# Performance work log

Hardware: AMD Instinct MI355X
Metric: run time of the kernel (lower is better)

The kernel has to match this reference:

```python
import jax, jax.numpy as jnp
import numpy as np

N = 100000      # nodes
E = 1600000     # edges (before self-loops)
IN = 256        # in_channels
H = 4           # heads (layer 1)
C = 16          # hidden_channels
OUT = 40        # out_channels
NEG_SLOPE = 0.2  # PyG GATConv default


def setup_inputs() -> dict:
    key = jax.random.key(0)
    ks = jax.random.split(key, 10)
    x = jax.random.normal(ks[0], (N, IN), dtype=jnp.float32)
    edge_index = jax.random.randint(ks[1], (2, E), 0, N, dtype=jnp.int64)
    s = 0.1
    return {
        "x": x,
        "edge_index": edge_index,
        "W1": jax.random.normal(ks[2], (IN, H * C), dtype=jnp.float32) * s,
        "a_src1": jax.random.normal(ks[3], (H, C), dtype=jnp.float32) * s,
        "a_dst1": jax.random.normal(ks[4], (H, C), dtype=jnp.float32) * s,
        "b1": jnp.zeros((H * C,), dtype=jnp.float32),
        "W2": jax.random.normal(ks[5], (H * C, OUT), dtype=jnp.float32) * s,
        "a_src2": jax.random.normal(ks[6], (1, OUT), dtype=jnp.float32) * s,
        "a_dst2": jax.random.normal(ks[7], (1, OUT), dtype=jnp.float32) * s,
        "b2": jnp.zeros((OUT,), dtype=jnp.float32),
    }


def gat_conv(x, src, dst, W, a_s, a_d, b, heads, ch, n):
    # x: [n, d_in] -> projected [n, heads, ch]
    xp = (x @ W).reshape(n, heads, ch)
    # per-node attention contributions [n, heads]
    e_s = jnp.einsum('nhc,hc->nh', xp, a_s)
    e_d = jnp.einsum('nhc,hc->nh', xp, a_d)
    # per-edge logits (gather) [E, heads]
    e = jax.nn.leaky_relu(e_s[src] + e_d[dst], negative_slope=NEG_SLOPE)
    # segment softmax over edges sharing a destination node
    m = jax.ops.segment_max(e, dst, num_segments=n)
    m = jnp.where(jnp.isfinite(m), m, 0.0)
    ex = jnp.exp(e - m[dst])
    z = jax.ops.segment_sum(ex, dst, num_segments=n)
    alpha = ex / (z[dst] + 1e-16)               # [E, heads]
    # weighted scatter-add aggregation [n, heads, ch]
    out = jax.ops.segment_sum(xp[src] * alpha[:, :, None], dst, num_segments=n)
    return out.reshape(n, heads * ch) + b       # concat heads + bias


def reference(x, edge_index, W1, a_src1, a_dst1, b1, W2, a_src2, a_dst2, b2):
    n = x.shape[0]
    loop = jnp.arange(n, dtype=edge_index.dtype)
    src = jnp.concatenate([edge_index[0], loop])  # PyG add_self_loops=True
    dst = jnp.concatenate([edge_index[1], loop])
    h = gat_conv(x, src, dst, W1, a_src1, a_dst1, b1, H, C, n)
    h = jax.nn.relu(h)
    out = gat_conv(h, src, dst, W2, a_src2, a_dst2, b2, 1, OUT, n)
    return out
```

## Files before the change

kernel.cpp:

```cpp
#include <hip/hip_runtime.h>
#include <hip/hip_bf16.h>

#define IN_DIM 256
#define HC     64
#define OUT_DIM 40
#define NEG    0.2f

#define NB_SH   8
#define NB_MASK 255
#define SRC_BITS 17
#define SRC_MASK 0x1FFFF
#define CHUNK   8192
#define LEN_CAP 6144

typedef __bf16 bf16x8 __attribute__((ext_vector_type(8)));
typedef float  f32x4  __attribute__((ext_vector_type(4)));

__device__ inline float lrelu(float v) { return fmaxf(v, NEG * v); }

__global__ __launch_bounds__(256) void hist_kernel(
    const int* __restrict__ ei, int* __restrict__ blkhistT, int* __restrict__ btot,
    int E, int ET, int nbuck, int nblk) {
  __shared__ int hist[512];
  int tid = threadIdx.x;
  hist[tid] = 0; hist[tid + 256] = 0;
  __syncthreads();
  int base = blockIdx.x * CHUNK;
  #pragma unroll
  for (int it = 0; it < CHUNK / 1024; ++it) {
    int e = base + it * 1024 + tid * 4;
    if (e + 3 < E) {
      int4 d4 = *(const int4*)&ei[E + e];
      atomicAdd(&hist[d4.x >> NB_SH], 1);
      atomicAdd(&hist[d4.y >> NB_SH], 1);
      atomicAdd(&hist[d4.z >> NB_SH], 1);
      atomicAdd(&hist[d4.w >> NB_SH], 1);
    } else {
      #pragma unroll
      for (int k = 0; k < 4; ++k) {
        int ee = e + k;
        if (ee < ET) {
          int d = (ee < E) ? ei[E + ee] : (ee - E);
          atomicAdd(&hist[d >> NB_SH], 1);
        }
      }
    }
  }
  __syncthreads();
  for (int i = tid; i < nbuck; i += 256) {
    int c = hist[i];
    blkhistT[(size_t)i * nblk + blockIdx.x] = c;
    if (c) atomicAdd(&btot[i], c);
  }
}

__global__ __launch_bounds__(512) void bscan_kernel(
    const int* __restrict__ btot, int* __restrict__ bstart,
    int* __restrict__ offs, int nbuck, int ET, int n) {
  __shared__ int sm[512];
  int tid = threadIdx.x;
  int total = (tid < nbuck) ? btot[tid] : 0;
  sm[tid] = total; __syncthreads();
  for (int o = 1; o < 512; o <<= 1) {
    int v = (tid >= o) ? sm[tid - o] : 0;
    __syncthreads();
    sm[tid] += v;
    __syncthreads();
  }
  if (tid < nbuck) bstart[tid] = sm[tid] - total;
  if (tid == 0) { bstart[nbuck] = ET; offs[n] = ET; }
}

__global__ __launch_bounds__(256) void curs_kernel(
    const int* __restrict__ blkhistT, const int* __restrict__ bstart,
    int* __restrict__ cur, int nblk, int nbuck) {
  __shared__ int sm[256];
  int b = blockIdx.x, tid = threadIdx.x;
  int run = bstart[b];
  for (int c = 0; c < nblk; c += 256) {
    int idx = c + tid;
    int v = (idx < nblk) ? blkhistT[(size_t)b * nblk + idx] : 0;
    sm[tid] = v; __syncthreads();
    for (int o = 1; o < 256; o <<= 1) {
      int x = (tid >= o) ? sm[tid - o] : 0;
      __syncthreads();
      sm[tid] += x;
      __syncthreads();
    }
    if (idx < nblk) cur[(size_t)idx * nbuck + b] = run + sm[tid] - v;
    run += sm[255];
    __syncthreads();
  }
}

__global__ __launch_bounds__(512) void scatter1_kernel(
    const int* __restrict__ ei, const int* __restrict__ cur,
    unsigned int* __restrict__ pairs, int E, int ET, int nbuck) {
  __shared__ int hs[512];
  __shared__ int addb[512];
  __shared__ int lcnt[512];
  __shared__ unsigned int lout[CHUNK];
  __shared__ int ldst[CHUNK];
  int tid = threadIdx.x, blk = blockIdx.x, base = blk * CHUNK;
  hs[tid] = 0; lcnt[tid] = 0;
  __syncthreads();
  int se[16], de[16];
  #pragma unroll
  for (int it = 0; it < CHUNK / 2048; ++it) {
    int e = base + it * 2048 + tid * 4;
    if (e + 3 < E) {
      int4 s4 = *(const int4*)&ei[e];
      int4 d4 = *(const int4*)&ei[E + e];
      se[it * 4 + 0] = s4.x; de[it * 4 + 0] = d4.x; atomicAdd(&hs[d4.x >> NB_SH], 1);
      se[it * 4 + 1] = s4.y; de[it * 4 + 1] = d4.y; atomicAdd(&hs[d4.y >> NB_SH], 1);
      se[it * 4 + 2] = s4.z; de[it * 4 + 2] = d4.z; atomicAdd(&hs[d4.z >> NB_SH], 1);
      se[it * 4 + 3] = s4.w; de[it * 4 + 3] = d4.w; atomicAdd(&hs[d4.w >> NB_SH], 1);
    } else {
      #pragma unroll
      for (int k = 0; k < 4; ++k) {
        int ee = e + k;
        int s = 0, d = 0;
        if (ee < ET) {
          if (ee < E) { s = ei[ee]; d = ei[E + ee]; }
          else        { s = ee - E; d = s; }
          atomicAdd(&hs[d >> NB_SH], 1);
        }
        se[it * 4 + k] = s; de[it * 4 + k] = d;
      }
    }
  }
  __syncthreads();
  int t = hs[tid];
  for (int o = 1; o < 512; o <<= 1) {
    int v = (tid >= o) ? hs[tid - o] : 0;
    __syncthreads();
    hs[tid] += v;
    __syncthreads();
  }
  int lofs = hs[tid] - t;
  __syncthreads();
  hs[tid] = lofs;
  addb[tid] = ((tid < nbuck) ? cur[(size_t)blk * nbuck + tid] : 0) - lofs;
  __syncthreads();
  #pragma unroll
  for (int it = 0; it < CHUNK / 2048; ++it) {
    #pragma unroll
    for (int k = 0; k < 4; ++k) {
      int e = base + it * 2048 + tid * 4 + k;
      if (e < ET) {
        int b = de[it * 4 + k] >> NB_SH;
        int pos = hs[b] + atomicAdd(&lcnt[b], 1);
        lout[pos] = (unsigned)se[it * 4 + k] |
                    ((unsigned)(de[it * 4 + k] & NB_MASK) << SRC_BITS);
        ldst[pos] = addb[b] + pos;
      }
    }
  }
  __syncthreads();
  int len = min(CHUNK, ET - base);
  for (int i = tid; i < len; i += 512) pairs[ldst[i]] = lout[i];
}

__global__ __launch_bounds__(512) void place2_kernel(
    const unsigned int* __restrict__ pairs, const int* __restrict__ bstart,
    int* __restrict__ offs, int* __restrict__ srcs, int n, int nbuck) {
  __shared__ unsigned int lin[LEN_CAP];
  __shared__ unsigned int lou[LEN_CAP];
  __shared__ int lhs[256];
  __shared__ int lcnt[256];
  __shared__ int sm[512];
  int b = blockIdx.x, tid = threadIdx.x;
  int rbeg = bstart[b], rend = bstart[b + 1], len = rend - rbeg;
  int node0 = b << NB_SH;
  int nloc = min(256, n - node0);
  if (tid < 256) { lhs[tid] = 0; lcnt[tid] = 0; }
  __syncthreads();
  if (len <= LEN_CAP) {
    for (int i = tid; i < len; i += 512) {
      unsigned p = pairs[rbeg + i];
      lin[i] = p;
      atomicAdd(&lhs[(p >> SRC_BITS) & NB_MASK], 1);
    }
    __syncthreads();
    int t = (tid < 256) ? lhs[tid] : 0;
    sm[tid] = t; __syncthreads();
    for (int o = 1; o < 512; o <<= 1) {
      int v = (tid >= o) ? sm[tid - o] : 0;
      __syncthreads();
      sm[tid] += v;
      __syncthreads();
    }
    int excl = sm[tid] - t;
    if (tid < nloc) offs[node0 + tid] = rbeg + excl;
    if (tid < 256) lhs[tid] = excl;
    __syncthreads();
    for (int i = tid; i < len; i += 512) {
      unsigned p = lin[i];
      int dl = (p >> SRC_BITS) & NB_MASK;
      int pos = lhs[dl] + atomicAdd(&lcnt[dl], 1);
      lou[pos] = p & SRC_MASK;
    }
    __syncthreads();
    for (int i = tid; i < len; i += 512) srcs[rbeg + i] = (int)lou[i];
  } else {
    for (int i = tid; i < len; i += 512)
      atomicAdd(&lhs[(pairs[rbeg + i] >> SRC_BITS) & NB_MASK], 1);
    __syncthreads();
    int t = (tid < 256) ? lhs[tid] : 0;
    sm[tid] = t; __syncthreads();
    for (int o = 1; o < 512; o <<= 1) {
      int v = (tid >= o) ? sm[tid - o] : 0;
      __syncthreads();
      sm[tid] += v;
      __syncthreads();
    }
    int excl = sm[tid] - t;
    if (tid < nloc) offs[node0 + tid] = rbeg + excl;
    if (tid < 256) lhs[tid] = excl;
    __syncthreads();
    for (int i = tid; i < len; i += 512) {
      unsigned p = pairs[rbeg + i];
      int dl = (p >> SRC_BITS) & NB_MASK;
      int pos = lhs[dl] + atomicAdd(&lcnt[dl], 1);
      srcs[rbeg + pos] = (int)(p & SRC_MASK);
    }
  }
}

__global__ void wprep_kernel(const float* __restrict__ W1, __bf16* __restrict__ Wt,
                             int* __restrict__ btot, int nbuck) {
  int i = blockIdx.x * blockDim.x + threadIdx.x;
  if (i < nbuck) btot[i] = 0;
  if (i >= IN_DIM * HC) return;
  int k = i >> 6, nn = i & 63;
  Wt[nn * IN_DIM + k] = (__bf16)W1[i];
}

__global__ __launch_bounds__(256, 4) void gemm1_mfma(
    const float* __restrict__ x, const __bf16* __restrict__ Wt,
    const float* __restrict__ a_s, const float* __restrict__ a_d,
    __bf16* __restrict__ xp1b, float* __restrict__ es1, float* __restrict__ ed1, int n) {
  __shared__ uint4 wl[2048];
  int tid = threadIdx.x;
  const uint4* gw = (const uint4*)Wt;
  #pragma unroll
  for (int it = 0; it < 8; ++it) {
    int c16 = it * 256 + tid;
    int row = c16 >> 5;
    int swz = c16 ^ (row & 7);
    wl[swz] = gw[c16];
  }
  __syncthreads();

  int wave = tid >> 6, lane = tid & 63;
  int l15 = lane & 15, kgrp = lane >> 4;
  int rowA = blockIdx.x * 64 + wave * 16 + l15;
  bool okA = rowA < n;
  const float* xrow = x + (size_t)(okA ? rowA : (n - 1)) * IN_DIM;

  f32x4 va[8][2];
  #pragma unroll
  for (int c = 0; c < 8; ++c) {
    int k0 = c * 32 + kgrp * 8;
    va[c][0] = *(const f32x4*)(xrow + k0);
    va[c][1] = *(const f32x4*)(xrow + k0 + 4);
  }
  __builtin_amdgcn_sched_barrier(0);

  f32x4 acc[4] = {};
  #pragma unroll
  for (int c = 0; c < 8; ++c) {
    bf16x8 ahi, alo;
    #pragma unroll
    for (int i = 0; i < 4; ++i) {
      float f0 = va[c][0][i], f1 = va[c][1][i];
      __bf16 h0 = (__bf16)f0, h1 = (__bf16)f1;
      ahi[i]     = h0;
      ahi[4 + i] = h1;
      alo[i]     = (__bf16)(f0 - (float)h0);
      alo[4 + i] = (__bf16)(f1 - (float)h1);
    }
    #pragma unroll
    for (int t = 0; t < 4; ++t) {
      int row  = t * 16 + l15;
      int unit = row * 32 + c * 4 + kgrp;
      int swz  = unit ^ (row & 7);
      bf16x8 b = *(const bf16x8*)&wl[swz];
      acc[t] = __builtin_amdgcn_mfma_f32_16x16x32_bf16(ahi, b, acc[t], 0, 0, 0);
      acc[t] = __builtin_amdgcn_mfma_f32_16x16x32_bf16(alo, b, acc[t], 0, 0, 0);
    }
  }

  int rowbase = blockIdx.x * 64 + wave * 16 + kgrp * 4;
  #pragma unroll
  for (int t = 0; t < 4; ++t) {
    float as_v = a_s[t * 16 + l15], ad_v = a_d[t * 16 + l15];
    #pragma unroll
    for (int r = 0; r < 4; ++r) {
      int row = rowbase + r;
      float v = acc[t][r];
      bool ok = row < n;
      if (ok) xp1b[(size_t)row * HC + t * 16 + l15] = (__bf16)v;
      float ps = v * as_v, pd = v * ad_v;
      #pragma unroll
      for (int o = 1; o < 16; o <<= 1) {
        ps += __shfl_xor(ps, o, 16);
        pd += __shfl_xor(pd, o, 16);
      }
      if (ok && l15 == 0) {
        es1[row * 4 + t] = ps;
        ed1[row * 4 + t] = pd;
      }
    }
  }
}

__global__ __launch_bounds__(256) void agg1_csr(
    const int* __restrict__ offs, const int* __restrict__ srcs,
    const float* __restrict__ es1, const float* __restrict__ ed1,
    const __bf16* __restrict__ xp1b, const float* __restrict__ b1,
    __bf16* __restrict__ hb, int n) {
  __shared__ float lds[4][16 * 4 * 2];
  int wave = threadIdx.x >> 6;
  int wid = (blockIdx.x * 256 + threadIdx.x) >> 6;
  if (wid >= n) return;
  int lane = threadIdx.x & 63;
  int eidx = lane >> 2, hA = lane & 3;
  int a = lane & 31, half = lane >> 5;
  int ch0 = a * 2, headB = a >> 3;
  int beg = offs[wid], end = offs[wid + 1];
  float edh = ed1[wid * 4 + hA];
  float zacc = 0.f, acc0 = 0.f, acc1 = 0.f;
  const char* xbase = (const char*)xp1b + ch0 * 2;
  float* myl = lds[wave];

  for (int e0 = beg; e0 < end; e0 += 16) {
    int cnt = min(16, end - e0);
    float ex = 0.f;
    int s = 0;
    if (eidx < cnt) {
      s = srcs[e0 + eidx];
      ex = __expf(lrelu(es1[s * 4 + hA] + edh));
    }
    zacc += ex;
    myl[lane * 2]     = ex;
    myl[lane * 2 + 1] = __int_as_float(s * (int)(HC * sizeof(__bf16)));
    if (cnt == 16) {
      float2 ao[8];
      #pragma unroll
      for (int jp = 0; jp < 8; ++jp)
        ao[jp] = *(const float2*)&myl[((jp * 2 + half) * 4 + headB) * 2];
      unsigned wj[8];
      #pragma unroll
      for (int jp = 0; jp < 8; ++jp)
        wj[jp] = *(const unsigned*)(xbase + __float_as_int(ao[jp].y));
      #pragma unroll
      for (int jp = 0; jp < 8; ++jp) {
        float f0 = __int_as_float((int)(wj[jp] << 16));
        float f1 = __int_as_float((int)(wj[jp] & 0xffff0000u));
        acc0 = fmaf(ao[jp].x, f0, acc0);
        acc1 = fmaf(ao[jp].x, f1, acc1);
      }
    } else {
      int jpmax = (cnt + 1 - half) >> 1;
      #pragma unroll 4
      for (int jp = 0; jp < jpmax; ++jp) {
        float2 ao = *(const float2*)&myl[((jp * 2 + half) * 4 + headB) * 2];
        unsigned w = *(const unsigned*)(xbase + __float_as_int(ao.y));
        float f0 = __int_as_float((int)(w << 16));
        float f1 = __int_as_float((int)(w & 0xffff0000u));
        acc0 = fmaf(ao.x, f0, acc0);
        acc1 = fmaf(ao.x, f1, acc1);
      }
    }
  }

  float z = zacc;
  z += __shfl_xor(z, 4); z += __shfl_xor(z, 8);
  z += __shfl_xor(z, 16); z += __shfl_xor(z, 32);
  float zc = __shfl(z, headB);
  acc0 += __shfl_xor(acc0, 32);
  acc1 += __shfl_xor(acc1, 32);
  if (half == 0) {
    float inv = 1.f / (zc + 1e-16f);
    __bf16 r0 = (__bf16)fmaxf(fmaf(acc0, inv, b1[ch0]), 0.f);
    __bf16 r1 = (__bf16)fmaxf(fmaf(acc1, inv, b1[ch0 + 1]), 0.f);
    unsigned pk = ((unsigned)*(unsigned short*)&r0) |
                  (((unsigned)*(unsigned short*)&r1) << 16);
    *(unsigned*)&hb[(size_t)wid * HC + ch0] = pk;
  }
}

__global__ __launch_bounds__(256) void layer2_mfma(
    const __bf16* __restrict__ hb, const float* __restrict__ W2,
    const float* __restrict__ a_s2, const float* __restrict__ a_d2,
    __bf16* __restrict__ xp2b, float* __restrict__ es2, float* __restrict__ ed2, int n) {
  int tid = threadIdx.x;
  int wave = tid >> 6, lane = tid & 63;
  int l15 = lane & 15, kgrp = lane >> 4;
  int rowA = blockIdx.x * 64 + wave * 16 + l15;
  const __bf16* hrow = hb + (size_t)(rowA < n ? rowA : (n - 1)) * HC;

  bf16x8 av[2];
  av[0] = *(const bf16x8*)(hrow + kgrp * 8);
  av[1] = *(const bf16x8*)(hrow + 32 + kgrp * 8);

  f32x4 acc[3] = {};
  #pragma unroll
  for (int c = 0; c < 2; ++c) {
    #pragma unroll
    for (int t = 0; t < 3; ++t) {
      int col = t * 16 + l15;
      bool okc = col < OUT_DIM;
      bf16x8 bhi, blo;
      #pragma unroll
      for (int i = 0; i < 8; ++i) {
        int k = c * 32 + kgrp * 8 + i;
        float w = okc ? W2[k * OUT_DIM + col] : 0.f;
        __bf16 wh = (__bf16)w;
        bhi[i] = wh;
        blo[i] = (__bf16)(w - (float)wh);
      }
      acc[t] = __builtin_amdgcn_mfma_f32_16x16x32_bf16(av[c], bhi, acc[t], 0, 0, 0);
      acc[t] = __builtin_amdgcn_mfma_f32_16x16x32_bf16(av[c], blo, acc[t], 0, 0, 0);
    }
  }

  int rowbase = blockIdx.x * 64 + wave * 16 + kgrp * 4;
  #pragma unroll
  for (int r = 0; r < 4; ++r) {
    int row = rowbase + r;
    bool ok = row < n;
    float ps = 0.f, pd = 0.f;
    #pragma unroll
    for (int t = 0; t < 3; ++t) {
      int col = t * 16 + l15;
      if (col < OUT_DIM) {
        float v = acc[t][r];
        if (ok) xp2b[(size_t)row * OUT_DIM + col] = (__bf16)v;
        ps = fmaf(v, a_s2[col], ps);
        pd = fmaf(v, a_d2[col], pd);
      }
    }
    #pragma unroll
    for (int o = 1; o < 16; o <<= 1) {
      ps += __shfl_xor(ps, o, 16);
      pd += __shfl_xor(pd, o, 16);
    }
    if (ok && l15 == 0) { es2[row] = ps; ed2[row] = pd; }
  }
}

__global__ __launch_bounds__(256) void agg2_csr(
    const int* __restrict__ offs, const int* __restrict__ srcs,
    const float* __restrict__ es2, const float* __restrict__ ed2,
    const __bf16* __restrict__ xp2b, const float* __restrict__ b2,
    float* __restrict__ out, int n) {
  __shared__ float lds[4][64 * 2];
  int wave = threadIdx.x >> 6;
  int wid = (blockIdx.x * 256 + threadIdx.x) >> 6;
  if (wid >= n) return;
  int lane = threadIdx.x & 63;
  int a = lane & 31, half = lane >> 5;
  int ch0 = a * 2;
  int beg = offs[wid], end = offs[wid + 1];
  float edv = ed2[wid];
  float zacc = 0.f, acc0 = 0.f, acc1 = 0.f;
  const char* xbase = (const char*)xp2b + ch0 * 2;
  float* myl = lds[wave];

  for (int e0 = beg; e0 < end; e0 += 64) {
    int cnt = min(64, end - e0);
    float ex = 0.f;
    int s = 0;
    if (lane < cnt) {
      s = srcs[e0 + lane];
      ex = __expf(lrelu(es2[s] + edv));
    }
    zacc += ex;
    myl[lane * 2]     = ex;
    myl[lane * 2 + 1] = __int_as_float(s * (int)(OUT_DIM * sizeof(__bf16)));
    if (a < 20) {
      int jpmax = (cnt + 1 - half) >> 1;
      int jp = 0;
      for (; jp + 8 <= jpmax; jp += 8) {
        float2 ao[8];
        #pragma unroll
        for (int k = 0; k < 8; ++k)
          ao[k] = *(const float2*)&myl[((jp + k) * 2 + half) * 2];
        unsigned wj[8];
        #pragma unroll
        for (int k = 0; k < 8; ++k)
          wj[k] = *(const unsigned*)(xbase + __float_as_int(ao[k].y));
        #pragma unroll
        for (int k = 0; k < 8; ++k) {
          float f0 = __int_as_float((int)(wj[k] << 16));
          float f1 = __int_as_float((int)(wj[k] & 0xffff0000u));
          acc0 = fmaf(ao[k].x, f0, acc0);
          acc1 = fmaf(ao[k].x, f1, acc1);
        }
      }
      #pragma unroll 4
      for (; jp < jpmax; ++jp) {
        float2 ao = *(const float2*)&myl[(jp * 2 + half) * 2];
        unsigned w = *(const unsigned*)(xbase + __float_as_int(ao.y));
        float f0 = __int_as_float((int)(w << 16));
        float f1 = __int_as_float((int)(w & 0xffff0000u));
        acc0 = fmaf(ao.x, f0, acc0);
        acc1 = fmaf(ao.x, f1, acc1);
      }
    }
  }

  float z = zacc;
  #pragma unroll
  for (int o = 1; o < 64; o <<= 1) z += __shfl_xor(z, o);
  acc0 += __shfl_xor(acc0, 32);
  acc1 += __shfl_xor(acc1, 32);
  if (half == 0 && a < 20) {
    float inv = 1.f / (z + 1e-16f);
    float2 r;
    r.x = fmaf(acc0, inv, b2[ch0]);
    r.y = fmaf(acc1, inv, b2[ch0 + 1]);
    *(float2*)&out[(size_t)wid * OUT_DIM + ch0] = r;
  }
}

extern "C" void kernel_launch(void* const* d_in, const int* in_sizes, int n_in,
                              void* d_out, int out_size, void* d_ws, size_t ws_size,
                              hipStream_t stream) {
  const float* x    = (const float*)d_in[0];
  const int*   ei   = (const int*)d_in[1];
  const float* W1   = (const float*)d_in[2];
  const float* a_s1 = (const float*)d_in[3];
  const float* a_d1 = (const float*)d_in[4];
  const float* b1   = (const float*)d_in[5];
  const float* W2   = (const float*)d_in[6];
  const float* a_s2 = (const float*)d_in[7];
  const float* a_d2 = (const float*)d_in[8];
  const float* b2   = (const float*)d_in[9];

  int n  = in_sizes[0] / IN_DIM;
  int E  = in_sizes[1] / 2;
  int ET = E + n;
  int nbuck = (n + 255) >> NB_SH;
  int nblk1 = (ET + CHUNK - 1) / CHUNK;
  float* out = (float*)d_out;

  char* ws = (char*)d_ws;
  size_t off = 0;
  auto alloc = [&](size_t bytes) -> void* {
    void* p = ws + off;
    off = (off + bytes + 255) & ~(size_t)255;
    return p;
  };
  __bf16* xp1b     = (__bf16*)alloc((size_t)n * HC * 2);
  __bf16* xp2b     = (__bf16*)alloc((size_t)n * OUT_DIM * 2);
  __bf16* hb       = (__bf16*)alloc((size_t)n * HC * 2);
  float*  es1      = (float*)alloc((size_t)n * 4 * 4);
  float*  ed1      = (float*)alloc((size_t)n * 4 * 4);
  float*  es2      = (float*)alloc((size_t)n * 4);
  float*  ed2      = (float*)alloc((size_t)n * 4);
  int*    blkhistT = (int*)alloc((size_t)nblk1 * nbuck * 4);
  int*    cur      = (int*)alloc((size_t)nblk1 * nbuck * 4);
  int*    btot     = (int*)alloc((size_t)(nbuck + 1) * 4);
  int*    bstart   = (int*)alloc((size_t)(nbuck + 1) * 4);
  int*    offs     = (int*)alloc((size_t)(n + 1) * 4);
  int*    srcs     = (int*)alloc((size_t)ET * 4);
  unsigned int* pairs = (unsigned int*)alloc((size_t)ET * 4);
  __bf16* Wt       = (__bf16*)alloc((size_t)IN_DIM * HC * 2);

  wprep_kernel<<<(IN_DIM * HC + 255) / 256, 256, 0, stream>>>(W1, Wt, btot, nbuck);
  hist_kernel<<<nblk1, 256, 0, stream>>>(ei, blkhistT, btot, E, ET, nbuck, nblk1);
  bscan_kernel<<<1, 512, 0, stream>>>(btot, bstart, offs, nbuck, ET, n);
  curs_kernel<<<nbuck, 256, 0, stream>>>(blkhistT, bstart, cur, nblk1, nbuck);
  scatter1_kernel<<<nblk1, 512, 0, stream>>>(ei, cur, pairs, E, ET, nbuck);
  place2_kernel<<<nbuck, 512, 0, stream>>>(pairs, bstart, offs, srcs, n, nbuck);

  gemm1_mfma<<<(n + 63) / 64, 256, 0, stream>>>(x, Wt, a_s1, a_d1,
                                                xp1b, es1, ed1, n);
  agg1_csr<<<(n * 64 + 255) / 256, 256, 0, stream>>>(offs, srcs, es1, ed1, xp1b, b1, hb, n);
  layer2_mfma<<<(n + 63) / 64, 256, 0, stream>>>(hb, W2, a_s2, a_d2, xp2b, es2, ed2, n);
  agg2_csr<<<(n * 64 + 255) / 256, 256, 0, stream>>>(offs, srcs, es2, ed2, xp2b, b2, out, n);
}
```

Baseline: 194.9 us.

## Co-schedule layer-1 GEMM tiles with CSR scatter and place kernels

The layer-1 projection GEMM no longer runs as its own kernel. Its tiles are split in half and appended as extra blocks to the scatter and place kernels, so the compute-bound MFMA work can overlap the memory-bound CSR construction. The GEMM now uses 512-thread blocks over 128-row tiles, and each kernel carves its shared memory out of one union buffer. The large shared footprint (about 70 KB) limits occupancy for both roles, and the GEMM blocks lose the launch_bounds(256,4) tuning they had before.

Measured after the change: 185.7 us (median of 2 runs). 4.7% less time.

```diff
diff --git a/kernel.cpp b/kernel.cpp
--- a/kernel.cpp
+++ b/kernel.cpp
@@ -93,14 +93,102 @@
   }
 }
 
-__global__ __launch_bounds__(512) void scatter1_kernel(
+__device__ __forceinline__ void gemm1_body(
+    char* smem, int tile,
+    const float* __restrict__ x, const __bf16* __restrict__ Wt,
+    const float* __restrict__ a_s, const float* __restrict__ a_d,
+    __bf16* __restrict__ xp1b, float* __restrict__ es1, float* __restrict__ ed1, int n) {
+  uint4* wl = (uint4*)smem;
+  int tid = threadIdx.x;
+  const uint4* gw = (const uint4*)Wt;
+  #pragma unroll
+  for (int it = 0; it < 4; ++it) {
+    int c16 = it * 512 + tid;
+    int row = c16 >> 5;
+    int swz = c16 ^ (row & 7);
+    wl[swz] = gw[c16];
+  }
+  __syncthreads();
+
+  int wave = tid >> 6, lane = tid & 63;
+  int l15 = lane & 15, kgrp = lane >> 4;
+  int rowA = tile * 128 + wave * 16 + l15;
+  bool okA = rowA < n;
+  const float* xrow = x + (size_t)(okA ? rowA : (n - 1)) * IN_DIM;
+
+  f32x4 va[8][2];
+  #pragma unroll
+  for (int c = 0; c < 8; ++c) {
+    int k0 = c * 32 + kgrp * 8;
+    va[c][0] = *(const f32x4*)(xrow + k0);
+    va[c][1] = *(const f32x4*)(xrow + k0 + 4);
+  }
+  __builtin_amdgcn_sched_barrier(0);
+
+  f32x4 acc[4] = {};
+  #pragma unroll
+  for (int c = 0; c < 8; ++c) {
+    bf16x8 ahi, alo;
+    #pragma unroll
+    for (int i = 0; i < 4; ++i) {
+      float f0 = va[c][0][i], f1 = va[c][1][i];
+      __bf16 h0 = (__bf16)f0, h1 = (__bf16)f1;
+      ahi[i]     = h0;
+      ahi[4 + i] = h1;
+      alo[i]     = (__bf16)(f0 - (float)h0);
+      alo[4 + i] = (__bf16)(f1 - (float)h1);
+    }
+    #pragma unroll
+    for (int t = 0; t < 4; ++t) {
+      int row  = t * 16 + l15;
+      int unit = row * 32 + c * 4 + kgrp;
+      int swz  = unit ^ (row & 7);
+      bf16x8 b = *(const bf16x8*)&wl[swz];
+      acc[t] = __builtin_amdgcn_mfma_f32_16x16x32_bf16(ahi, b, acc[t], 0, 0, 0);
+      acc[t] = __builtin_amdgcn_mfma_f32_16x16x32_bf16(alo, b, acc[t], 0, 0, 0);
+    }
+  }
+
+  int rowbase = tile * 128 + wave * 16 + kgrp * 4;
+  #pragma unroll
+  for (int t = 0; t < 4; ++t) {
+    float as_v = a_s[t * 16 + l15], ad_v = a_d[t * 16 + l15];
+    #pragma unroll
+    for (int r = 0; r < 4; ++r) {
+      int row = rowbase + r;
+      float v = acc[t][r];
+      bool ok = row < n;
+      if (ok) xp1b[(size_t)row * HC + t * 16 + l15] = (__bf16)v;
+      float ps = v * as_v, pd = v * ad_v;
+      #pragma unroll
+      for (int o = 1; o < 16; o <<= 1) {
+        ps += __shfl_xor(ps, o, 16);
+        pd += __shfl_xor(pd, o, 16);
+      }
+      if (ok && l15 == 0) {
+        es1[row * 4 + t] = ps;
+        ed1[row * 4 + t] = pd;
+      }
+    }
+  }
+}
+
+__global__ __launch_bounds__(512) void fused_sg(
     const int* __restrict__ ei, const int* __restrict__ cur,
-    unsigned int* __restrict__ pairs, int E, int ET, int nbuck) {
-  __shared__ int hs[512];
-  __shared__ int addb[512];
-  __shared__ int lcnt[512];
-  __shared__ unsigned int lout[CHUNK];
-  __shared__ int ldst[CHUNK];
+    unsigned int* __restrict__ pairs, int E, int ET, int nbuck, int nsc,
+    const float* __restrict__ x, const __bf16* __restrict__ Wt,
+    const float* __restrict__ a_s, const float* __restrict__ a_d,
+    __bf16* __restrict__ xp1b, float* __restrict__ es1, float* __restrict__ ed1, int n) {
+  __shared__ __align__(16) char smem[71680];
+  if ((int)blockIdx.x >= nsc) {
+    gemm1_body(smem, (int)blockIdx.x - nsc, x, Wt, a_s, a_d, xp1b, es1, ed1, n);
+    return;
+  }
+  int* hs   = (int*)smem;
+  int* addb = (int*)(smem + 2048);
+  int* lcnt = (int*)(smem + 4096);
+  unsigned int* lout = (unsigned int*)(smem + 6144);
+  int* ldst = (int*)(smem + 6144 + CHUNK * 4);
   int tid = threadIdx.x, blk = blockIdx.x, base = blk * CHUNK;
   hs[tid] = 0; lcnt[tid] = 0;
   __syncthreads();
@@ -161,14 +249,22 @@
   for (int i = tid; i < len; i += 512) pairs[ldst[i]] = lout[i];
 }
 
-__global__ __launch_bounds__(512) void place2_kernel(
+__global__ __launch_bounds__(512) void fused_pg(
     const unsigned int* __restrict__ pairs, const int* __restrict__ bstart,
-    int* __restrict__ offs, int* __restrict__ srcs, int n, int nbuck) {
-  __shared__ unsigned int lin[LEN_CAP];
-  __shared__ unsigned int lou[LEN_CAP];
-  __shared__ int lhs[256];
-  __shared__ int lcnt[256];
-  __shared__ int sm[512];
+    int* __restrict__ offs, int* __restrict__ srcs, int n, int nbuck, int tile0,
+    const float* __restrict__ x, const __bf16* __restrict__ Wt,
+    const float* __restrict__ a_s, const float* __restrict__ a_d,
+    __bf16* __restrict__ xp1b, float* __restrict__ es1, float* __restrict__ ed1) {
+  __shared__ __align__(16) char smem[53248];
+  if ((int)blockIdx.x >= nbuck) {
+    gemm1_body(smem, tile0 + (int)blockIdx.x - nbuck, x, Wt, a_s, a_d, xp1b, es1, ed1, n);
+    return;
+  }
+  unsigned int* lin = (unsigned int*)smem;
+  unsigned int* lou = (unsigned int*)(smem + 24576);
+  int* lhs  = (int*)(smem + 49152);
+  int* lcnt = (int*)(smem + 50176);
+  int* sm   = (int*)(smem + 51200);
   int b = blockIdx.x, tid = threadIdx.x;
   int rbeg = bstart[b], rend = bstart[b + 1], len = rend - rbeg;
   int node0 = b << NB_SH;
@@ -234,85 +330,6 @@
   if (i >= IN_DIM * HC) return;
   int k = i >> 6, nn = i & 63;
   Wt[nn * IN_DIM + k] = (__bf16)W1[i];
-}
-
-__global__ __launch_bounds__(256, 4) void gemm1_mfma(
-    const float* __restrict__ x, const __bf16* __restrict__ Wt,
-    const float* __restrict__ a_s, const float* __restrict__ a_d,
-    __bf16* __restrict__ xp1b, float* __restrict__ es1, float* __restrict__ ed1, int n) {
-  __shared__ uint4 wl[2048];
-  int tid = threadIdx.x;
-  const uint4* gw = (const uint4*)Wt;
-  #pragma unroll
-  for (int it = 0; it < 8; ++it) {
-    int c16 = it * 256 + tid;
-    int row = c16 >> 5;
-    int swz = c16 ^ (row & 7);
-    wl[swz] = gw[c16];
-  }
-  __syncthreads();
-
-  int wave = tid >> 6, lane = tid & 63;
-  int l15 = lane & 15, kgrp = lane >> 4;
-  int rowA = blockIdx.x * 64 + wave * 16 + l15;
-  bool okA = rowA < n;
-  const float* xrow = x + (size_t)(okA ? rowA : (n - 1)) * IN_DIM;
-
-  f32x4 va[8][2];
-  #pragma unroll
-  for (int c = 0; c < 8; ++c) {
-    int k0 = c * 32 + kgrp * 8;
-    va[c][0] = *(const f32x4*)(xrow + k0);
-    va[c][1] = *(const f32x4*)(xrow + k0 + 4);
-  }
-  __builtin_amdgcn_sched_barrier(0);
-
-  f32x4 acc[4] = {};
-  #pragma unroll
-  for (int c = 0; c < 8; ++c) {
-    bf16x8 ahi, alo;
-    #pragma unroll
-    for (int i = 0; i < 4; ++i) {
-      float f0 = va[c][0][i], f1 = va[c][1][i];
-      __bf16 h0 = (__bf16)f0, h1 = (__bf16)f1;
-      ahi[i]     = h0;
-      ahi[4 + i] = h1;
-      alo[i]     = (__bf16)(f0 - (float)h0);
-      alo[4 + i] = (__bf16)(f1 - (float)h1);
-    }
-    #pragma unroll
-    for (int t = 0; t < 4; ++t) {
-      int row  = t * 16 + l15;
-      int unit = row * 32 + c * 4 + kgrp;
-      int swz  = unit ^ (row & 7);
-      bf16x8 b = *(const bf16x8*)&wl[swz];
-      acc[t] = __builtin_amdgcn_mfma_f32_16x16x32_bf16(ahi, b, acc[t], 0, 0, 0);
-      acc[t] = __builtin_amdgcn_mfma_f32_16x16x32_bf16(alo, b, acc[t], 0, 0, 0);
-    }
-  }
-
-  int rowbase = blockIdx.x * 64 + wave * 16 + kgrp * 4;
-  #pragma unroll
-  for (int t = 0; t < 4; ++t) {
-    float as_v = a_s[t * 16 + l15], ad_v = a_d[t * 16 + l15];
-    #pragma unroll
-    for (int r = 0; r < 4; ++r) {
-      int row = rowbase + r;
-      float v = acc[t][r];
-      bool ok = row < n;
-      if (ok) xp1b[(size_t)row * HC + t * 16 + l15] = (__bf16)v;
-      float ps = v * as_v, pd = v * ad_v;
-      #pragma unroll
-      for (int o = 1; o < 16; o <<= 1) {
-        ps += __shfl_xor(ps, o, 16);
-        pd += __shfl_xor(pd, o, 16);
-      }
-      if (ok && l15 == 0) {
-        es1[row * 4 + t] = ps;
-        ed1[row * 4 + t] = pd;
-      }
-    }
-  }
 }
 
 __global__ __launch_bounds__(256) void agg1_csr(
@@ -545,6 +562,8 @@
   int ET = E + n;
   int nbuck = (n + 255) >> NB_SH;
   int nblk1 = (ET + CHUNK - 1) / CHUNK;
+  int ntile = (n + 127) / 128;
+  int t0 = ntile / 2;
   float* out = (float*)d_out;
 
   char* ws = (char*)d_ws;
@@ -574,11 +593,10 @@
   hist_kernel<<<nblk1, 256, 0, stream>>>(ei, blkhistT, btot, E, ET, nbuck, nblk1);
   bscan_kernel<<<1, 512, 0, stream>>>(btot, bstart, offs, nbuck, ET, n);
   curs_kernel<<<nbuck, 256, 0, stream>>>(blkhistT, bstart, cur, nblk1, nbuck);
-  scatter1_kernel<<<nblk1, 512, 0, stream>>>(ei, cur, pairs, E, ET, nbuck);
-  place2_kernel<<<nbuck, 512, 0, stream>>>(pairs, bstart, offs, srcs, n, nbuck);
-
-  gemm1_mfma<<<(n + 63) / 64, 256, 0, stream>>>(x, Wt, a_s1, a_d1,
-                                                xp1b, es1, ed1, n);
+  fused_sg<<<nblk1 + t0, 512, 0, stream>>>(ei, cur, pairs, E, ET, nbuck, nblk1,
+                                           x, Wt, a_s1, a_d1, xp1b, es1, ed1, n);
+  fused_pg<<<nbuck + (ntile - t0), 512, 0, stream>>>(pairs, bstart, offs, srcs, n, nbuck, t0,
+                                                     x, Wt, a_s1, a_d1, xp1b, es1, ed1);
   agg1_csr<<<(n * 64 + 255) / 256, 256, 0, stream>>>(offs, srcs, es1, ed1, xp1b, b1, hb, n);
   layer2_mfma<<<(n + 63) / 64, 256, 0, stream>>>(hb, W2, a_s2, a_d2, xp2b, es2, ed2, n);
   agg2_csr<<<(n * 64 + 255) / 256, 256, 0, stream>>>(offs, srcs, es2, ed2, xp2b, b2, out, n);
```
